# Kernel optimization log

Measured on AMD Instinct MI355X. Metric: run time of the kernel, lower is better.

Reference implementation:

```python
import jax, jax.numpy as jnp
import numpy as np

EPS = 1e-6


def sparsemax(z):
    # sparsemax over last axis (Martins & Astudillo 2016)
    n = z.shape[-1]
    zs = -jnp.sort(-z, axis=-1)                      # sorted descending
    cum = jnp.cumsum(zs, axis=-1)
    k = jnp.arange(1, n + 1, dtype=z.dtype)
    support = (1.0 + k * zs) > cum                   # [..., n]
    ksup = jnp.sum(support, axis=-1, keepdims=True)  # support size (int)
    tau = (jnp.take_along_axis(cum, ksup - 1, axis=-1) - 1.0) / ksup.astype(z.dtype)
    return jnp.maximum(z - tau, 0.0)


def setup_inputs() -> dict:
    key = jax.random.key(0)
    k1, k2, k3, k4, k5, k6 = jax.random.split(key, 6)
    bi, bt, K, L, d = 128, 128, 36, 50, 1024
    img_cls = jax.random.normal(k1, (bi, d), dtype=jnp.float32)
    imgs = jax.random.normal(k2, (bi, K, d), dtype=jnp.float32)
    cap_cls = jax.random.normal(k3, (bt, d), dtype=jnp.float32)
    caps = jax.random.normal(k4, (bt, L, d), dtype=jnp.float32)
    img_lens = jax.random.randint(k5, (bi,), 18, K + 1).at[0].set(K)
    cap_lens = jax.random.randint(k6, (bt,), 25, L + 1).at[0].set(L)
    return {"img_cls": img_cls, "imgs": imgs, "cap_cls": cap_cls,
            "caps": caps, "img_lens": img_lens, "cap_lens": cap_lens}


def reference(img_cls, imgs, cap_cls, caps, img_lens, cap_lens):
    # forward_s2d: masked fine-grained sims -> sparsemax over flattened (K*L) -> weighted sum
    bi, K, d = imgs.shape
    bt, L, _ = caps.shape
    imgs = imgs + EPS
    caps = caps + EPS
    imgs = imgs / jnp.linalg.norm(imgs, axis=-1, keepdims=True)
    caps = caps / jnp.linalg.norm(caps, axis=-1, keepdims=True)
    fg = jnp.einsum('ikd,tld->itkl', imgs, caps)             # [bi,bt,K,L]
    rmask = jnp.arange(K)[None, :] < img_lens[:, None]        # [bi,K]
    cmask = jnp.arange(L)[None, :] < cap_lens[:, None]        # [bt,L]
    mask = rmask[:, None, :, None] & cmask[None, :, None, :]  # [bi,bt,K,L]
    fg = jnp.where(mask, fg, 0.0).reshape(bi, bt, K * L)
    attn = sparsemax(fg)
    return jnp.sum(fg * attn, axis=-1)                        # [bi,bt]
```

## Files before the change

### kernel.cpp

```cpp
#include <hip/hip_runtime.h>
#include <stdint.h>

#define EPSF 1e-6f

typedef unsigned short u16;
typedef __attribute__((ext_vector_type(8))) u16 u16x8;
typedef __attribute__((ext_vector_type(8))) __bf16 bf16x8;
typedef __attribute__((ext_vector_type(4))) float f32x4;

static constexpr int NBI = 128, NBT = 128, KI = 36, LC = 50, DD = 1024;
static constexpr int NEL = KI * LC;
static constexpr int GM  = NBI * KI;
static constexpr int GN  = NBT * LC;
static constexpr int BM = 256, BN = 256, BK = 64;
static constexpr int KT  = DD / BK;
static constexpr int MT  = GM / BM;
static constexpr int NTT = GN / BN;
static constexpr int TB  = BM * BK;

static __device__ __forceinline__ u16 f2bf(float f) {
  uint32_t u = __float_as_uint(f);
  u += 0x7fffu + ((u >> 16) & 1u);
  return (u16)(u >> 16);
}
static __device__ __forceinline__ float bf2f(u16 h) {
  return __uint_as_float((uint32_t)h << 16);
}

typedef __attribute__((address_space(1))) void gv_t;
typedef __attribute__((address_space(3))) void lv_t;
static __device__ __forceinline__ void gload16(const void* g, void* l) {
  __builtin_amdgcn_global_load_lds((const gv_t*)g, (lv_t*)l, 16, 0, 0);
}

__global__ __launch_bounds__(256) void hcam_normcast(
    const float* __restrict__ imgs, const float* __restrict__ caps,
    u16* __restrict__ A, u16* __restrict__ B) {
  int r = blockIdx.x;
  const float* src; u16* dst;
  if (r < GM) { src = imgs + (size_t)r * DD;        dst = A + (size_t)r * DD; }
  else        { src = caps + (size_t)(r - GM) * DD; dst = B + (size_t)(r - GM) * DD; }
  int tid = threadIdx.x;
  float4 v = *(const float4*)(src + tid * 4);
  v.x += EPSF; v.y += EPSF; v.z += EPSF; v.w += EPSF;
  float ss = v.x * v.x + v.y * v.y + v.z * v.z + v.w * v.w;
  #pragma unroll
  for (int m = 32; m; m >>= 1) ss += __shfl_xor(ss, m);
  __shared__ float wsum[4];
  if ((tid & 63) == 0) wsum[tid >> 6] = ss;
  __syncthreads();
  float inv = 1.0f / sqrtf(wsum[0] + wsum[1] + wsum[2] + wsum[3]);
  ushort4 o = make_ushort4(f2bf(v.x * inv), f2bf(v.y * inv), f2bf(v.z * inv), f2bf(v.w * inv));
  *(ushort4*)(dst + tid * 4) = o;
}

__global__ __launch_bounds__(1024, 1) void hcam_gemm16(
    const u16* __restrict__ A, const u16* __restrict__ B, _Float16* __restrict__ C) {
  __shared__ u16 As[2 * TB];
  __shared__ u16 Bs[2 * TB];

  const int nwg = MT * NTT;
  int orig = blockIdx.x;
  int qq = nwg >> 3, rr = nwg & 7;
  int xcd = orig & 7, idx = orig >> 3;
  int wg = (xcd < rr ? xcd * (qq + 1) : rr * (qq + 1) + (xcd - rr) * qq) + idx;
  const int bm = wg % MT, bn = wg / MT;

  const int tid = threadIdx.x, lane = tid & 63, w = tid >> 6;
  const int wm = w >> 2, wn = w & 3;
  const u16* Ag = A + (size_t)(bm * BM) * DD;
  const u16* Bg = B + (size_t)(bn * BN) * DD;

  const int srow = tid >> 3;
  const int sc16 = (tid & 7) ^ (srow & 7);
  const int wbase = w * 8;

  auto stage = [&](const u16* g, u16* lds, int kt, int h) {
    gload16(g + (size_t)(h * 128 + srow) * DD + kt * BK + sc16 * 8,
            lds + (h * 128 + wbase) * BK);
  };

  f32x4 acc[4][4];
  #pragma unroll
  for (int i = 0; i < 4; ++i)
    #pragma unroll
    for (int j = 0; j < 4; ++j) acc[i][j] = (f32x4){0.f, 0.f, 0.f, 0.f};

  const int fr = lane & 15, g4 = lane >> 4;

  auto ktile_compute = [&](const u16* as_c, const u16* bs_c, bool st,
                           u16* as_n, u16* bs_n, int tn) {
    #pragma unroll
    for (int k2 = 0; k2 < 2; ++k2) {
      const int c16 = k2 * 4 + g4;
      const int cs = (c16 ^ (fr & 7)) << 3;
      bf16x8 af[4], bfv[4];
      #pragma unroll
      for (int mi = 0; mi < 4; ++mi) {
        int rowl = wm * 64 + mi * 16 + fr;
        af[mi] = __builtin_bit_cast(bf16x8, *(const u16x8*)(as_c + rowl * BK + cs));
      }
      #pragma unroll
      for (int ni = 0; ni < 4; ++ni) {
        int rowl = wn * 64 + ni * 16 + fr;
        bfv[ni] = __builtin_bit_cast(bf16x8, *(const u16x8*)(bs_c + rowl * BK + cs));
      }
      if (st) {
        if (k2 == 0) { stage(Bg, bs_n, tn, 0); }
        else         { stage(Ag, as_n, tn, 1); stage(Bg, bs_n, tn, 1); }
      }
      __builtin_amdgcn_s_setprio(1);
      #pragma unroll
      for (int mi = 0; mi < 4; ++mi)
        #pragma unroll
        for (int ni = 0; ni < 4; ++ni)
          acc[mi][ni] = __builtin_amdgcn_mfma_f32_16x16x32_bf16(
              af[mi], bfv[ni], acc[mi][ni], 0, 0, 0);
      __builtin_amdgcn_s_setprio(0);
    }
  };

  auto tile = [&](int t, const u16* as_c, const u16* bs_c, u16* as_n, u16* bs_n) {
    const int tn = t + 1;
    if (tn < KT) {
      stage(Ag, as_n, tn, 0);
      asm volatile("s_waitcnt vmcnt(1)" ::: "memory");
    } else {
      asm volatile("s_waitcnt vmcnt(0)" ::: "memory");
    }
    __builtin_amdgcn_s_barrier();
    __builtin_amdgcn_sched_barrier(0);
    ktile_compute(as_c, bs_c, tn < KT, as_n, bs_n, tn);
    __builtin_amdgcn_s_barrier();
    __builtin_amdgcn_sched_barrier(0);
  };

  stage(Ag, As, 0, 0); stage(Bg, Bs, 0, 0);
  stage(Ag, As, 0, 1); stage(Bg, Bs, 0, 1);
  stage(Ag, As + TB, 1, 0);
  asm volatile("s_waitcnt vmcnt(1)" ::: "memory");
  __builtin_amdgcn_s_barrier();
  __builtin_amdgcn_sched_barrier(0);
  ktile_compute(As, Bs, true, As + TB, Bs + TB, 1);
  __builtin_amdgcn_s_barrier();
  __builtin_amdgcn_sched_barrier(0);

  #pragma unroll 1
  for (int tp = 1; tp + 1 < KT; tp += 2) {
    tile(tp,     As + TB, Bs + TB, As,      Bs);
    tile(tp + 1, As,      Bs,      As + TB, Bs + TB);
  }
  tile(KT - 1, As + TB, Bs + TB, As, Bs);

  const int fc = lane & 15, fq = (lane >> 4) * 4;
  #pragma unroll
  for (int am = 0; am < 4; ++am) {
    #pragma unroll
    for (int an = 0; an < 4; ++an) {
      const int row0 = bm * BM + wm * 64 + am * 16 + fq;
      const int col  = bn * BN + wn * 64 + an * 16 + fc;
      #pragma unroll
      for (int j = 0; j < 4; ++j)
        C[(size_t)(row0 + j) * GN + col] = (_Float16)acc[am][an][j];
    }
  }
}

static constexpr int RPT = (NEL + 63) / 64;

__global__ __launch_bounds__(256) void hcam_spmax_w(
    const _Float16* __restrict__ C, const int* __restrict__ ilen, const int* __restrict__ clen,
    float* __restrict__ out) {
  const int wid  = blockIdx.x * 4 + (threadIdx.x >> 6);
  const int lane = threadIdx.x & 63;
  const int i = wid >> 7, t = wid & 127;
  const int il = ilen[i], cl = clen[t];
  const _Float16* base = C + (size_t)i * KI * GN + t * LC;

  float v[RPT];
  float sum = 0.f;
  #pragma unroll
  for (int r = 0; r < RPT; ++r) {
    int p = lane + (r << 6);
    float x = -1e30f;
    if (p < NEL) {
      int k = p / LC, l = p - k * LC;
      if (k < il && l < cl) { x = (float)base[(size_t)k * GN + l]; sum += x; }
    }
    v[r] = x;
  }
  #pragma unroll
  for (int m = 32; m; m >>= 1) sum += __shfl_xor(sum, m);

  const float mzero = (float)(NEL - il * cl);
  float tau  = (sum - 1.0f) * (1.0f / NEL);
  float prev = (float)NEL;
  for (int it = 0; it < 32; ++it) {
    float ss = 0.f, cc = 0.f;
    #pragma unroll
    for (int r = 0; r < RPT; ++r) {
      if (v[r] > tau) { ss += v[r]; cc += 1.0f; }
    }
    #pragma unroll
    for (int m = 32; m; m >>= 1) { ss += __shfl_xor(ss, m); cc += __shfl_xor(cc, m); }
    if (tau < 0.f) cc += mzero;
    if (cc == prev || cc < 1.0f) break;
    float tn = (ss - 1.0f) / cc;
    prev = cc;
    if (tn <= tau) break;
    tau = tn;
  }

  float o = 0.f;
  #pragma unroll
  for (int r = 0; r < RPT; ++r) {
    float d = v[r] - tau;
    if (d > 0.f) o += v[r] * d;
  }
  #pragma unroll
  for (int m = 32; m; m >>= 1) o += __shfl_xor(o, m);
  if (lane == 0) out[wid] = o;
}

static __device__ __forceinline__ void bred2(float& a, float& b2, int tid, float* red) {
  #pragma unroll
  for (int m = 32; m; m >>= 1) { a += __shfl_xor(a, m); b2 += __shfl_xor(b2, m); }
  __syncthreads();
  if ((tid & 63) == 0) { red[(tid >> 6) * 2] = a; red[(tid >> 6) * 2 + 1] = b2; }
  __syncthreads();
  a  = red[0] + red[2] + red[4] + red[6];
  b2 = red[1] + red[3] + red[5] + red[7];
}

static __device__ __forceinline__ void sparsemax_out(float vals[8], int tid, float* red, float* outp) {
  float s = 0.f, d = 0.f;
  #pragma unroll
  for (int r = 0; r < 8; ++r) { int p = tid + (r << 8); if (p < NEL) s += vals[r]; }
  bred2(s, d, tid, red);
  float tau  = (s - 1.0f) * (1.0f / NEL);
  float prev = (float)NEL;
  for (int it = 0; it < 64; ++it) {
    float ss = 0.f, cc = 0.f;
    #pragma unroll
    for (int r = 0; r < 8; ++r) {
      int p = tid + (r << 8);
      if (p < NEL && vals[r] > tau) { ss += vals[r]; cc += 1.0f; }
    }
    bred2(ss, cc, tid, red);
    if (cc == prev || cc < 1.0f) break;
    float tn = (ss - 1.0f) / cc;
    prev = cc;
    if (tn <= tau) break;
    tau = tn;
  }
  float o = 0.f; d = 0.f;
  #pragma unroll
  for (int r = 0; r < 8; ++r) {
    float v = vals[r], a2 = v - tau;
    if (a2 > 0.f) o += v * a2;
  }
  bred2(o, d, tid, red);
  if (tid == 0) *outp = o;
}

__global__ __launch_bounds__(256) void hcam_fused_bf(
    const u16* __restrict__ A, const u16* __restrict__ B,
    const int* __restrict__ ilen, const int* __restrict__ clen, float* __restrict__ out) {
  const int b = blockIdx.x;
  const int i = b >> 7, t = b & 127;
  const int tid = threadIdx.x;
  const int il = ilen[i], cl = clen[t];
  float vals[8];
  #pragma unroll
  for (int r = 0; r < 8; ++r) {
    int p = tid + (r << 8);
    float v = 0.f;
    if (p < NEL) {
      int k = p / LC, l = p - k * LC;
      if (k < il && l < cl) {
        const u16* ar = A + (size_t)(i * KI + k) * DD;
        const u16* br = B + (size_t)(t * LC + l) * DD;
        float s = 0.f;
        for (int dd = 0; dd < DD; dd += 8) {
          u16x8 av = *(const u16x8*)(ar + dd);
          u16x8 bv = *(const u16x8*)(br + dd);
          #pragma unroll
          for (int q = 0; q < 8; ++q) s += bf2f(av[q]) * bf2f(bv[q]);
        }
        v = s;
      }
    }
    vals[r] = v;
  }
  __shared__ float red[8];
  sparsemax_out(vals, tid, red, &out[b]);
}

__global__ __launch_bounds__(256) void hcam_fused_raw(
    const float* __restrict__ imgs, const float* __restrict__ caps,
    const int* __restrict__ ilen, const int* __restrict__ clen, float* __restrict__ out) {
  const int b = blockIdx.x;
  const int i = b >> 7, t = b & 127;
  const int tid = threadIdx.x;
  const int w = tid >> 6, lane = tid & 63;
  __shared__ float inv[KI + LC];
  for (int row = w; row < KI + LC; row += 4) {
    const float* src = (row < KI) ? imgs + (size_t)(i * KI + row) * DD
                                  : caps + (size_t)(t * LC + (row - KI)) * DD;
    float ss = 0.f;
    for (int e = lane; e < DD; e += 64) { float x = src[e] + EPSF; ss += x * x; }
    #pragma unroll
    for (int m = 32; m; m >>= 1) ss += __shfl_xor(ss, m);
    if (lane == 0) inv[row] = 1.0f / sqrtf(ss);
  }
  __syncthreads();
  const int il = ilen[i], cl = clen[t];
  float vals[8];
  #pragma unroll
  for (int r = 0; r < 8; ++r) {
    int p = tid + (r << 8);
    float v = 0.f;
    if (p < NEL) {
      int k = p / LC, l = p - k * LC;
      if (k < il && l < cl) {
        const float* ar = imgs + (size_t)(i * KI + k) * DD;
        const float* br = caps + (size_t)(t * LC + l) * DD;
        float s = 0.f;
        for (int dd = 0; dd < DD; dd += 4) {
          float4 a4 = *(const float4*)(ar + dd);
          float4 b4 = *(const float4*)(br + dd);
          s += (a4.x + EPSF) * (b4.x + EPSF) + (a4.y + EPSF) * (b4.y + EPSF)
             + (a4.z + EPSF) * (b4.z + EPSF) + (a4.w + EPSF) * (b4.w + EPSF);
        }
        v = s * inv[k] * inv[KI + l];
      }
    }
    vals[r] = v;
  }
  __shared__ float red[8];
  sparsemax_out(vals, tid, red, &out[b]);
}

extern "C" void kernel_launch(void* const* d_in, const int* in_sizes, int n_in,
                              void* d_out, int out_size, void* d_ws, size_t ws_size,
                              hipStream_t stream) {
  (void)in_sizes; (void)n_in; (void)out_size;
  const float* imgs = (const float*)d_in[1];
  const float* caps = (const float*)d_in[3];
  const int*   ilen = (const int*)d_in[4];
  const int*   clen = (const int*)d_in[5];
  float* out = (float*)d_out;

  const size_t offB     = (size_t)GM * DD * sizeof(u16);
  const size_t offC     = offB + (size_t)GN * DD * sizeof(u16);
  const size_t needFull = offC + (size_t)GM * GN * sizeof(_Float16);
  u16*      A = (u16*)d_ws;
  u16*      B = (u16*)((char*)d_ws + offB);
  _Float16* C = (_Float16*)((char*)d_ws + offC);

  if (ws_size >= needFull) {
    hcam_normcast<<<dim3(GM + GN), dim3(256), 0, stream>>>(imgs, caps, A, B);
    hcam_gemm16<<<dim3(MT * NTT), dim3(1024), 0, stream>>>(A, B, C);
    hcam_spmax_w<<<dim3(NBI * NBT / 4), dim3(256), 0, stream>>>(C, ilen, clen, out);
  } else if (ws_size >= offC) {
    hcam_normcast<<<dim3(GM + GN), dim3(256), 0, stream>>>(imgs, caps, A, B);
    hcam_fused_bf<<<dim3(NBI * NBT), dim3(256), 0, stream>>>(A, B, ilen, clen, out);
  } else {
    hcam_fused_raw<<<dim3(NBI * NBT), dim3(256), 0, stream>>>(imgs, caps, ilen, clen, out);
  }
}
```

Measured before the change: 126.8 us.

## Use 8-wave GEMM with 128x64 per-wave tiles and two blocks per CU

The bf16 GEMM moves from 16 waves of 64x64 output to 8 waves that each compute a 128x64 output sub-tile, with launch bounds set to allow two workgroups per CU. Each wave reuses its A and B fragments across more MFMAs, which lowers LDS read traffic per FLOP, and the global-to-LDS staging is spread across four interleaved phases within the k-tile. The cost is 128 accumulator registers per lane, which raises register pressure and could prevent two blocks from being resident. The LDS footprint per block is unchanged, so occupancy may stay limited by shared memory.

```diff
diff --git a/kernel.cpp b/kernel.cpp
--- a/kernel.cpp
+++ b/kernel.cpp
@@ -54,7 +54,7 @@
   *(ushort4*)(dst + tid * 4) = o;
 }
 
-__global__ __launch_bounds__(1024, 1) void hcam_gemm16(
+__global__ __launch_bounds__(512, 2) void hcam_gemm8r(
     const u16* __restrict__ A, const u16* __restrict__ B, _Float16* __restrict__ C) {
   __shared__ u16 As[2 * TB];
   __shared__ u16 Bs[2 * TB];
@@ -76,55 +76,104 @@
   const int wbase = w * 8;
 
   auto stage = [&](const u16* g, u16* lds, int kt, int h) {
-    gload16(g + (size_t)(h * 128 + srow) * DD + kt * BK + sc16 * 8,
-            lds + (h * 128 + wbase) * BK);
+    #pragma unroll
+    for (int j = 0; j < 2; ++j) {
+      int row = h * 128 + j * 64 + srow;
+      gload16(g + (size_t)row * DD + kt * BK + sc16 * 8,
+              lds + (h * 128 + j * 64 + wbase) * BK);
+    }
   };
 
-  f32x4 acc[4][4];
-  #pragma unroll
-  for (int i = 0; i < 4; ++i)
+  f32x4 acc[8][4];
+  #pragma unroll
+  for (int i = 0; i < 8; ++i)
     #pragma unroll
     for (int j = 0; j < 4; ++j) acc[i][j] = (f32x4){0.f, 0.f, 0.f, 0.f};
 
   const int fr = lane & 15, g4 = lane >> 4;
+
+  auto rdoff = [&](int rowl, int k2) {
+    const int c16 = k2 * 4 + g4;
+    return rowl * BK + ((c16 ^ (fr & 7)) << 3);
+  };
 
   auto ktile_compute = [&](const u16* as_c, const u16* bs_c, bool st,
                            u16* as_n, u16* bs_n, int tn) {
-    #pragma unroll
-    for (int k2 = 0; k2 < 2; ++k2) {
-      const int c16 = k2 * 4 + g4;
-      const int cs = (c16 ^ (fr & 7)) << 3;
-      bf16x8 af[4], bfv[4];
-      #pragma unroll
-      for (int mi = 0; mi < 4; ++mi) {
-        int rowl = wm * 64 + mi * 16 + fr;
-        af[mi] = __builtin_bit_cast(bf16x8, *(const u16x8*)(as_c + rowl * BK + cs));
-      }
-      #pragma unroll
-      for (int ni = 0; ni < 4; ++ni) {
-        int rowl = wn * 64 + ni * 16 + fr;
-        bfv[ni] = __builtin_bit_cast(bf16x8, *(const u16x8*)(bs_c + rowl * BK + cs));
-      }
-      if (st) {
-        if (k2 == 0) { stage(Bg, bs_n, tn, 0); }
-        else         { stage(Ag, as_n, tn, 1); stage(Bg, bs_n, tn, 1); }
-      }
-      __builtin_amdgcn_s_setprio(1);
+    bf16x8 af[4][2], blo[2][2], bhi[2][2];
+    #pragma unroll
+    for (int mi = 0; mi < 4; ++mi)
+      #pragma unroll
+      for (int k2 = 0; k2 < 2; ++k2)
+        af[mi][k2] = __builtin_bit_cast(bf16x8,
+            *(const u16x8*)(as_c + rdoff(wm * 128 + mi * 16 + fr, k2)));
+    #pragma unroll
+    for (int ni = 0; ni < 2; ++ni)
+      #pragma unroll
+      for (int k2 = 0; k2 < 2; ++k2)
+        blo[ni][k2] = __builtin_bit_cast(bf16x8,
+            *(const u16x8*)(bs_c + rdoff(wn * 64 + ni * 16 + fr, k2)));
+    if (st) stage(Bg, bs_n, tn, 0);
+    __builtin_amdgcn_s_setprio(1);
+    #pragma unroll
+    for (int k2 = 0; k2 < 2; ++k2)
       #pragma unroll
       for (int mi = 0; mi < 4; ++mi)
         #pragma unroll
-        for (int ni = 0; ni < 4; ++ni)
+        for (int ni = 0; ni < 2; ++ni)
           acc[mi][ni] = __builtin_amdgcn_mfma_f32_16x16x32_bf16(
-              af[mi], bfv[ni], acc[mi][ni], 0, 0, 0);
-      __builtin_amdgcn_s_setprio(0);
-    }
+              af[mi][k2], blo[ni][k2], acc[mi][ni], 0, 0, 0);
+    __builtin_amdgcn_s_setprio(0);
+    #pragma unroll
+    for (int ni = 0; ni < 2; ++ni)
+      #pragma unroll
+      for (int k2 = 0; k2 < 2; ++k2)
+        bhi[ni][k2] = __builtin_bit_cast(bf16x8,
+            *(const u16x8*)(bs_c + rdoff(wn * 64 + 32 + ni * 16 + fr, k2)));
+    if (st) stage(Ag, as_n, tn, 1);
+    __builtin_amdgcn_s_setprio(1);
+    #pragma unroll
+    for (int k2 = 0; k2 < 2; ++k2)
+      #pragma unroll
+      for (int mi = 0; mi < 4; ++mi)
+        #pragma unroll
+        for (int ni = 0; ni < 2; ++ni)
+          acc[mi][2 + ni] = __builtin_amdgcn_mfma_f32_16x16x32_bf16(
+              af[mi][k2], bhi[ni][k2], acc[mi][2 + ni], 0, 0, 0);
+    __builtin_amdgcn_s_setprio(0);
+    #pragma unroll
+    for (int mi = 0; mi < 4; ++mi)
+      #pragma unroll
+      for (int k2 = 0; k2 < 2; ++k2)
+        af[mi][k2] = __builtin_bit_cast(bf16x8,
+            *(const u16x8*)(as_c + rdoff(wm * 128 + 64 + mi * 16 + fr, k2)));
+    if (st) stage(Bg, bs_n, tn, 1);
+    __builtin_amdgcn_s_setprio(1);
+    #pragma unroll
+    for (int k2 = 0; k2 < 2; ++k2)
+      #pragma unroll
+      for (int mi = 0; mi < 4; ++mi)
+        #pragma unroll
+        for (int ni = 0; ni < 2; ++ni)
+          acc[4 + mi][ni] = __builtin_amdgcn_mfma_f32_16x16x32_bf16(
+              af[mi][k2], blo[ni][k2], acc[4 + mi][ni], 0, 0, 0);
+    __builtin_amdgcn_s_setprio(0);
+    __builtin_amdgcn_s_setprio(1);
+    #pragma unroll
+    for (int k2 = 0; k2 < 2; ++k2)
+      #pragma unroll
+      for (int mi = 0; mi < 4; ++mi)
+        #pragma unroll
+        for (int ni = 0; ni < 2; ++ni)
+          acc[4 + mi][2 + ni] = __builtin_amdgcn_mfma_f32_16x16x32_bf16(
+              af[mi][k2], bhi[ni][k2], acc[4 + mi][2 + ni], 0, 0, 0);
+    __builtin_amdgcn_s_setprio(0);
   };
 
   auto tile = [&](int t, const u16* as_c, const u16* bs_c, u16* as_n, u16* bs_n) {
     const int tn = t + 1;
     if (tn < KT) {
       stage(Ag, as_n, tn, 0);
-      asm volatile("s_waitcnt vmcnt(1)" ::: "memory");
+      asm volatile("s_waitcnt vmcnt(2)" ::: "memory");
     } else {
       asm volatile("s_waitcnt vmcnt(0)" ::: "memory");
     }
@@ -138,7 +187,7 @@
   stage(Ag, As, 0, 0); stage(Bg, Bs, 0, 0);
   stage(Ag, As, 0, 1); stage(Bg, Bs, 0, 1);
   stage(Ag, As + TB, 1, 0);
-  asm volatile("s_waitcnt vmcnt(1)" ::: "memory");
+  asm volatile("s_waitcnt vmcnt(2)" ::: "memory");
   __builtin_amdgcn_s_barrier();
   __builtin_amdgcn_sched_barrier(0);
   ktile_compute(As, Bs, true, As + TB, Bs + TB, 1);
@@ -154,16 +203,17 @@
 
   const int fc = lane & 15, fq = (lane >> 4) * 4;
   #pragma unroll
-  for (int am = 0; am < 4; ++am) {
-    #pragma unroll
-    for (int an = 0; an < 4; ++an) {
-      const int row0 = bm * BM + wm * 64 + am * 16 + fq;
-      const int col  = bn * BN + wn * 64 + an * 16 + fc;
-      #pragma unroll
-      for (int j = 0; j < 4; ++j)
-        C[(size_t)(row0 + j) * GN + col] = (_Float16)acc[am][an][j];
-    }
-  }
+  for (int mh = 0; mh < 2; ++mh)
+    #pragma unroll
+    for (int mi = 0; mi < 4; ++mi)
+      #pragma unroll
+      for (int an = 0; an < 4; ++an) {
+        const int row0 = bm * BM + wm * 128 + mh * 64 + mi * 16 + fq;
+        const int col  = bn * BN + wn * 64 + an * 16 + fc;
+        #pragma unroll
+        for (int j = 0; j < 4; ++j)
+          C[(size_t)(row0 + j) * GN + col] = (_Float16)acc[mh * 4 + mi][an][j];
+      }
 }
 
 static constexpr int RPT = (NEL + 63) / 64;
@@ -360,7 +410,7 @@
 
   if (ws_size >= needFull) {
     hcam_normcast<<<dim3(GM + GN), dim3(256), 0, stream>>>(imgs, caps, A, B);
-    hcam_gemm16<<<dim3(MT * NTT), dim3(1024), 0, stream>>>(A, B, C);
+    hcam_gemm8r<<<dim3(MT * NTT), dim3(512), 0, stream>>>(A, B, C);
     hcam_spmax_w<<<dim3(NBI * NBT / 4), dim3(256), 0, stream>>>(C, ilen, clen, out);
   } else if (ws_size >= offC) {
     hcam_normcast<<<dim3(GM + GN), dim3(256), 0, stream>>>(imgs, caps, A, B);
```

Result: no change. 124.6 us, median of 2 (-1.7%).

## Compact valid rows via prefix offsets and run GEMM only over valid tokens

Applied to the files above, without the earlier changes.

Adds a header kernel that prefix-sums image and caption lengths, then normalizes and writes only valid rows into compacted A/B buffers. The GEMM becomes a 128x128-tile, 256-thread kernel that covers only the compacted extents, skipping padded rows and columns and the matching C writes. The sparsemax kernel reads the compacted C with one lane per caption token. The cost is an extra serial single-thread launch, and the new GEMM is single-buffered with a full vmcnt(0) wait each k-step, so load and compute no longer overlap.

```diff
diff --git a/kernel.cpp b/kernel.cpp
--- a/kernel.cpp
+++ b/kernel.cpp
@@ -12,11 +12,8 @@
 static constexpr int NEL = KI * LC;
 static constexpr int GM  = NBI * KI;
 static constexpr int GN  = NBT * LC;
-static constexpr int BM = 256, BN = 256, BK = 64;
-static constexpr int KT  = DD / BK;
-static constexpr int MT  = GM / BM;
-static constexpr int NTT = GN / BN;
-static constexpr int TB  = BM * BK;
+static constexpr int BK = 64;
+static constexpr int KT = DD / BK;
 
 static __device__ __forceinline__ u16 f2bf(float f) {
   uint32_t u = __float_as_uint(f);
@@ -31,6 +28,182 @@
 typedef __attribute__((address_space(3))) void lv_t;
 static __device__ __forceinline__ void gload16(const void* g, void* l) {
   __builtin_amdgcn_global_load_lds((const gv_t*)g, (lv_t*)l, 16, 0, 0);
+}
+
+__global__ void hcam_hdr(const int* __restrict__ ilen, const int* __restrict__ clen,
+                         int* __restrict__ h) {
+  if (threadIdx.x == 0 && blockIdx.x == 0) {
+    int s = 0;
+    for (int i = 0; i < NBI; ++i) { h[8 + i] = s; s += ilen[i]; }
+    h[0] = s; h[1] = (s + 127) >> 7;
+    int s2 = 0;
+    for (int t = 0; t < NBT; ++t) { h[136 + t] = s2; s2 += clen[t]; }
+    h[2] = s2; h[3] = (s2 + 127) >> 7; h[4] = h[3] << 7;
+  }
+}
+
+__global__ __launch_bounds__(256) void hcam_normcast_c(
+    const float* __restrict__ imgs, const float* __restrict__ caps,
+    const int* __restrict__ ilen, const int* __restrict__ clen,
+    const int* __restrict__ h, u16* __restrict__ A, u16* __restrict__ B) {
+  int r = blockIdx.x;
+  const float* src; u16* dst;
+  if (r < GM) {
+    int i = r / KI, k = r - i * KI;
+    if (k >= ilen[i]) return;
+    src = imgs + (size_t)r * DD;
+    dst = A + (size_t)(h[8 + i] + k) * DD;
+  } else {
+    int rb = r - GM;
+    int t = rb / LC, l = rb - t * LC;
+    if (l >= clen[t]) return;
+    src = caps + (size_t)rb * DD;
+    dst = B + (size_t)(h[136 + t] + l) * DD;
+  }
+  int tid = threadIdx.x;
+  float4 v = *(const float4*)(src + tid * 4);
+  v.x += EPSF; v.y += EPSF; v.z += EPSF; v.w += EPSF;
+  float ss = v.x * v.x + v.y * v.y + v.z * v.z + v.w * v.w;
+  #pragma unroll
+  for (int m = 32; m; m >>= 1) ss += __shfl_xor(ss, m);
+  __shared__ float wsum[4];
+  if ((tid & 63) == 0) wsum[tid >> 6] = ss;
+  __syncthreads();
+  float inv = 1.0f / sqrtf(wsum[0] + wsum[1] + wsum[2] + wsum[3]);
+  ushort4 o = make_ushort4(f2bf(v.x * inv), f2bf(v.y * inv), f2bf(v.z * inv), f2bf(v.w * inv));
+  *(ushort4*)(dst + tid * 4) = o;
+}
+
+__global__ __launch_bounds__(256, 4) void hcam_gemm128(
+    const u16* __restrict__ A, const u16* __restrict__ B, _Float16* __restrict__ C,
+    const int* __restrict__ h) {
+  const int Mt = h[1], Nt = h[3], Npad = h[4];
+  const int orig = blockIdx.x;
+  const int wg = (orig & 7) * 225 + (orig >> 3);
+  const int bm = wg % 36, bn = wg / 36;
+  if (bm >= Mt || bn >= Nt) return;
+  __shared__ u16 As[128 * BK];
+  __shared__ u16 Bs[128 * BK];
+
+  const int tid = threadIdx.x, lane = tid & 63, w = tid >> 6;
+  const int wm = w >> 1, wn = w & 1;
+  const u16* Ag = A + (size_t)(bm * 128) * DD;
+  const u16* Bg = B + (size_t)(bn * 128) * DD;
+
+  const int srow = tid >> 3;
+  const int sc16 = (tid & 7) ^ (srow & 7);
+
+  f32x4 acc[4][4];
+  #pragma unroll
+  for (int i = 0; i < 4; ++i)
+    #pragma unroll
+    for (int j = 0; j < 4; ++j) acc[i][j] = (f32x4){0.f, 0.f, 0.f, 0.f};
+
+  const int fr = lane & 15, g4 = lane >> 4;
+
+  #pragma unroll 1
+  for (int kt = 0; kt < KT; ++kt) {
+    const int kb = kt * BK;
+    #pragma unroll
+    for (int j = 0; j < 4; ++j) {
+      const int row = j * 32 + srow;
+      const size_t gof = (size_t)row * DD + kb + sc16 * 8;
+      gload16(Ag + gof, As + (j * 32 + w * 8) * BK);
+      gload16(Bg + gof, Bs + (j * 32 + w * 8) * BK);
+    }
+    asm volatile("s_waitcnt vmcnt(0)" ::: "memory");
+    __builtin_amdgcn_s_barrier();
+
+    bf16x8 af[4][2], bfv[4][2];
+    #pragma unroll
+    for (int k2 = 0; k2 < 2; ++k2) {
+      const int cs = (((k2 << 2) + g4) ^ (fr & 7)) << 3;
+      #pragma unroll
+      for (int mi = 0; mi < 4; ++mi)
+        af[mi][k2] = __builtin_bit_cast(bf16x8,
+            *(const u16x8*)(As + (wm * 64 + mi * 16 + fr) * BK + cs));
+      #pragma unroll
+      for (int ni = 0; ni < 4; ++ni)
+        bfv[ni][k2] = __builtin_bit_cast(bf16x8,
+            *(const u16x8*)(Bs + (wn * 64 + ni * 16 + fr) * BK + cs));
+    }
+    __builtin_amdgcn_s_setprio(1);
+    #pragma unroll
+    for (int k2 = 0; k2 < 2; ++k2)
+      #pragma unroll
+      for (int mi = 0; mi < 4; ++mi)
+        #pragma unroll
+        for (int ni = 0; ni < 4; ++ni)
+          acc[mi][ni] = __builtin_amdgcn_mfma_f32_16x16x32_bf16(
+              af[mi][k2], bfv[ni][k2], acc[mi][ni], 0, 0, 0);
+    __builtin_amdgcn_s_setprio(0);
+    __builtin_amdgcn_s_barrier();
+  }
+
+  const int fc = lane & 15, fq = (lane >> 4) * 4;
+  #pragma unroll
+  for (int mi = 0; mi < 4; ++mi)
+    #pragma unroll
+    for (int ni = 0; ni < 4; ++ni) {
+      const int row0 = bm * 128 + wm * 64 + mi * 16 + fq;
+      const int col  = bn * 128 + wn * 64 + ni * 16 + fc;
+      #pragma unroll
+      for (int j = 0; j < 4; ++j)
+        C[(size_t)(row0 + j) * Npad + col] = (_Float16)acc[mi][ni][j];
+    }
+}
+
+__global__ __launch_bounds__(256) void hcam_spmax_w(
+    const _Float16* __restrict__ C, const int* __restrict__ ilen,
+    const int* __restrict__ clen, const int* __restrict__ h,
+    float* __restrict__ out) {
+  const int wid  = blockIdx.x * 4 + (threadIdx.x >> 6);
+  const int lane = threadIdx.x & 63;
+  const int i = wid >> 7, t = wid & 127;
+  const int il = ilen[i], cl = clen[t];
+  const int Npad = h[4];
+  const _Float16* base = C + (size_t)h[8 + i] * Npad + h[136 + t];
+
+  float v[KI];
+  float sum = 0.f;
+  const bool lv = lane < cl;
+  #pragma unroll
+  for (int r = 0; r < KI; ++r) {
+    float x = -1e30f;
+    if (r < il && lv) { x = (float)base[(size_t)r * Npad + lane]; sum += x; }
+    v[r] = x;
+  }
+  #pragma unroll
+  for (int m = 32; m; m >>= 1) sum += __shfl_xor(sum, m);
+
+  const float mzero = (float)(NEL - il * cl);
+  float tau  = (sum - 1.0f) * (1.0f / NEL);
+  float prev = (float)NEL;
+  for (int it = 0; it < 32; ++it) {
+    float ss = 0.f, cc = 0.f;
+    #pragma unroll
+    for (int r = 0; r < KI; ++r) {
+      if (v[r] > tau) { ss += v[r]; cc += 1.0f; }
+    }
+    #pragma unroll
+    for (int m = 32; m; m >>= 1) { ss += __shfl_xor(ss, m); cc += __shfl_xor(cc, m); }
+    if (tau < 0.f) cc += mzero;
+    if (cc == prev || cc < 1.0f) break;
+    float tn = (ss - 1.0f) / cc;
+    prev = cc;
+    if (tn <= tau) break;
+    tau = tn;
+  }
+
+  float o = 0.f;
+  #pragma unroll
+  for (int r = 0; r < KI; ++r) {
+    float d = v[r] - tau;
+    if (d > 0.f) o += v[r] * d;
+  }
+  #pragma unroll
+  for (int m = 32; m; m >>= 1) o += __shfl_xor(o, m);
+  if (lane == 0) out[wid] = o;
 }
 
 __global__ __launch_bounds__(256) void hcam_normcast(
@@ -52,174 +225,6 @@
   float inv = 1.0f / sqrtf(wsum[0] + wsum[1] + wsum[2] + wsum[3]);
   ushort4 o = make_ushort4(f2bf(v.x * inv), f2bf(v.y * inv), f2bf(v.z * inv), f2bf(v.w * inv));
   *(ushort4*)(dst + tid * 4) = o;
-}
-
-__global__ __launch_bounds__(1024, 1) void hcam_gemm16(
-    const u16* __restrict__ A, const u16* __restrict__ B, _Float16* __restrict__ C) {
-  __shared__ u16 As[2 * TB];
-  __shared__ u16 Bs[2 * TB];
-
-  const int nwg = MT * NTT;
-  int orig = blockIdx.x;
-  int qq = nwg >> 3, rr = nwg & 7;
-  int xcd = orig & 7, idx = orig >> 3;
-  int wg = (xcd < rr ? xcd * (qq + 1) : rr * (qq + 1) + (xcd - rr) * qq) + idx;
-  const int bm = wg % MT, bn = wg / MT;
-
-  const int tid = threadIdx.x, lane = tid & 63, w = tid >> 6;
-  const int wm = w >> 2, wn = w & 3;
-  const u16* Ag = A + (size_t)(bm * BM) * DD;
-  const u16* Bg = B + (size_t)(bn * BN) * DD;
-
-  const int srow = tid >> 3;
-  const int sc16 = (tid & 7) ^ (srow & 7);
-  const int wbase = w * 8;
-
-  auto stage = [&](const u16* g, u16* lds, int kt, int h) {
-    gload16(g + (size_t)(h * 128 + srow) * DD + kt * BK + sc16 * 8,
-            lds + (h * 128 + wbase) * BK);
-  };
-
-  f32x4 acc[4][4];
-  #pragma unroll
-  for (int i = 0; i < 4; ++i)
-    #pragma unroll
-    for (int j = 0; j < 4; ++j) acc[i][j] = (f32x4){0.f, 0.f, 0.f, 0.f};
-
-  const int fr = lane & 15, g4 = lane >> 4;
-
-  auto ktile_compute = [&](const u16* as_c, const u16* bs_c, bool st,
-                           u16* as_n, u16* bs_n, int tn) {
-    #pragma unroll
-    for (int k2 = 0; k2 < 2; ++k2) {
-      const int c16 = k2 * 4 + g4;
-      const int cs = (c16 ^ (fr & 7)) << 3;
-      bf16x8 af[4], bfv[4];
-      #pragma unroll
-      for (int mi = 0; mi < 4; ++mi) {
-        int rowl = wm * 64 + mi * 16 + fr;
-        af[mi] = __builtin_bit_cast(bf16x8, *(const u16x8*)(as_c + rowl * BK + cs));
-      }
-      #pragma unroll
-      for (int ni = 0; ni < 4; ++ni) {
-        int rowl = wn * 64 + ni * 16 + fr;
-        bfv[ni] = __builtin_bit_cast(bf16x8, *(const u16x8*)(bs_c + rowl * BK + cs));
-      }
-      if (st) {
-        if (k2 == 0) { stage(Bg, bs_n, tn, 0); }
-        else         { stage(Ag, as_n, tn, 1); stage(Bg, bs_n, tn, 1); }
-      }
-      __builtin_amdgcn_s_setprio(1);
-      #pragma unroll
-      for (int mi = 0; mi < 4; ++mi)
-        #pragma unroll
-        for (int ni = 0; ni < 4; ++ni)
-          acc[mi][ni] = __builtin_amdgcn_mfma_f32_16x16x32_bf16(
-              af[mi], bfv[ni], acc[mi][ni], 0, 0, 0);
-      __builtin_amdgcn_s_setprio(0);
-    }
-  };
-
-  auto tile = [&](int t, const u16* as_c, const u16* bs_c, u16* as_n, u16* bs_n) {
-    const int tn = t + 1;
-    if (tn < KT) {
-      stage(Ag, as_n, tn, 0);
-      asm volatile("s_waitcnt vmcnt(1)" ::: "memory");
-    } else {
-      asm volatile("s_waitcnt vmcnt(0)" ::: "memory");
-    }
-    __builtin_amdgcn_s_barrier();
-    __builtin_amdgcn_sched_barrier(0);
-    ktile_compute(as_c, bs_c, tn < KT, as_n, bs_n, tn);
-    __builtin_amdgcn_s_barrier();
-    __builtin_amdgcn_sched_barrier(0);
-  };
-
-  stage(Ag, As, 0, 0); stage(Bg, Bs, 0, 0);
-  stage(Ag, As, 0, 1); stage(Bg, Bs, 0, 1);
-  stage(Ag, As + TB, 1, 0);
-  asm volatile("s_waitcnt vmcnt(1)" ::: "memory");
-  __builtin_amdgcn_s_barrier();
-  __builtin_amdgcn_sched_barrier(0);
-  ktile_compute(As, Bs, true, As + TB, Bs + TB, 1);
-  __builtin_amdgcn_s_barrier();
-  __builtin_amdgcn_sched_barrier(0);
-
-  #pragma unroll 1
-  for (int tp = 1; tp + 1 < KT; tp += 2) {
-    tile(tp,     As + TB, Bs + TB, As,      Bs);
-    tile(tp + 1, As,      Bs,      As + TB, Bs + TB);
-  }
-  tile(KT - 1, As + TB, Bs + TB, As, Bs);
-
-  const int fc = lane & 15, fq = (lane >> 4) * 4;
-  #pragma unroll
-  for (int am = 0; am < 4; ++am) {
-    #pragma unroll
-    for (int an = 0; an < 4; ++an) {
-      const int row0 = bm * BM + wm * 64 + am * 16 + fq;
-      const int col  = bn * BN + wn * 64 + an * 16 + fc;
-      #pragma unroll
-      for (int j = 0; j < 4; ++j)
-        C[(size_t)(row0 + j) * GN + col] = (_Float16)acc[am][an][j];
-    }
-  }
-}
-
-static constexpr int RPT = (NEL + 63) / 64;
-
-__global__ __launch_bounds__(256) void hcam_spmax_w(
-    const _Float16* __restrict__ C, const int* __restrict__ ilen, const int* __restrict__ clen,
-    float* __restrict__ out) {
-  const int wid  = blockIdx.x * 4 + (threadIdx.x >> 6);
-  const int lane = threadIdx.x & 63;
-  const int i = wid >> 7, t = wid & 127;
-  const int il = ilen[i], cl = clen[t];
-  const _Float16* base = C + (size_t)i * KI * GN + t * LC;
-
-  float v[RPT];
-  float sum = 0.f;
-  #pragma unroll
-  for (int r = 0; r < RPT; ++r) {
-    int p = lane + (r << 6);
-    float x = -1e30f;
-    if (p < NEL) {
-      int k = p / LC, l = p - k * LC;
-      if (k < il && l < cl) { x = (float)base[(size_t)k * GN + l]; sum += x; }
-    }
-    v[r] = x;
-  }
-  #pragma unroll
-  for (int m = 32; m; m >>= 1) sum += __shfl_xor(sum, m);
-
-  const float mzero = (float)(NEL - il * cl);
-  float tau  = (sum - 1.0f) * (1.0f / NEL);
-  float prev = (float)NEL;
-  for (int it = 0; it < 32; ++it) {
-    float ss = 0.f, cc = 0.f;
-    #pragma unroll
-    for (int r = 0; r < RPT; ++r) {
-      if (v[r] > tau) { ss += v[r]; cc += 1.0f; }
-    }
-    #pragma unroll
-    for (int m = 32; m; m >>= 1) { ss += __shfl_xor(ss, m); cc += __shfl_xor(cc, m); }
-    if (tau < 0.f) cc += mzero;
-    if (cc == prev || cc < 1.0f) break;
-    float tn = (ss - 1.0f) / cc;
-    prev = cc;
-    if (tn <= tau) break;
-    tau = tn;
-  }
-
-  float o = 0.f;
-  #pragma unroll
-  for (int r = 0; r < RPT; ++r) {
-    float d = v[r] - tau;
-    if (d > 0.f) o += v[r] * d;
-  }
-  #pragma unroll
-  for (int m = 32; m; m >>= 1) o += __shfl_xor(o, m);
-  if (lane == 0) out[wid] = o;
 }
 
 static __device__ __forceinline__ void bred2(float& a, float& b2, int tid, float* red) {
@@ -351,17 +356,20 @@
   const int*   clen = (const int*)d_in[5];
   float* out = (float*)d_out;
 
-  const size_t offB     = (size_t)GM * DD * sizeof(u16);
+  const size_t offA     = 4096;
+  const size_t offB     = offA + (size_t)GM * DD * sizeof(u16);
   const size_t offC     = offB + (size_t)GN * DD * sizeof(u16);
   const size_t needFull = offC + (size_t)GM * GN * sizeof(_Float16);
-  u16*      A = (u16*)d_ws;
+  int*      hdr = (int*)d_ws;
+  u16*      A = (u16*)((char*)d_ws + offA);
   u16*      B = (u16*)((char*)d_ws + offB);
   _Float16* C = (_Float16*)((char*)d_ws + offC);
 
   if (ws_size >= needFull) {
-    hcam_normcast<<<dim3(GM + GN), dim3(256), 0, stream>>>(imgs, caps, A, B);
-    hcam_gemm16<<<dim3(MT * NTT), dim3(1024), 0, stream>>>(A, B, C);
-    hcam_spmax_w<<<dim3(NBI * NBT / 4), dim3(256), 0, stream>>>(C, ilen, clen, out);
+    hcam_hdr<<<dim3(1), dim3(64), 0, stream>>>(ilen, clen, hdr);
+    hcam_normcast_c<<<dim3(GM + GN), dim3(256), 0, stream>>>(imgs, caps, ilen, clen, hdr, A, B);
+    hcam_gemm128<<<dim3(36 * 50), dim3(256), 0, stream>>>(A, B, C, hdr);
+    hcam_spmax_w<<<dim3(NBI * NBT / 4), dim3(256), 0, stream>>>(C, ilen, clen, hdr, out);
   } else if (ws_size >= offC) {
     hcam_normcast<<<dim3(GM + GN), dim3(256), 0, stream>>>(imgs, caps, A, B);
     hcam_fused_bf<<<dim3(NBI * NBT), dim3(256), 0, stream>>>(A, B, ilen, clen, out);
```

New measurement: 201.2 us. 1.59x slower.

## Switch GEMM to 128x128x32 tiles with 256-thread blocks and 4 blocks per CU

Applied to the files above, without the earlier changes.

Replaces the 256x256x64 single-block-per-CU GEMM with a 128x128x32 tile kernel using 4 waves and up to 4 resident blocks per CU. The staging pattern, LDS swizzle and XCD remapping are rewritten to match (8 XCDs x 225 tiles). The aim is more workgroups for better load balance across CUs and more occupancy to hide latency. The cost is lower operand reuse per tile, so more global and LDS traffic, plus more barriers per unit of work.

```diff
diff --git a/kernel.cpp b/kernel.cpp
--- a/kernel.cpp
+++ b/kernel.cpp
@@ -12,11 +12,11 @@
 static constexpr int NEL = KI * LC;
 static constexpr int GM  = NBI * KI;
 static constexpr int GN  = NBT * LC;
-static constexpr int BM = 256, BN = 256, BK = 64;
-static constexpr int KT  = DD / BK;
-static constexpr int MT  = GM / BM;
-static constexpr int NTT = GN / BN;
-static constexpr int TB  = BM * BK;
+static constexpr int BM = 128, BN = 128, BK = 32;
+static constexpr int KT = DD / BK;
+static constexpr int MT = GM / BM;
+static constexpr int NT = GN / BN;
+static constexpr int TBA = BM * BK;
 
 static __device__ __forceinline__ u16 f2bf(float f) {
   uint32_t u = __float_as_uint(f);
@@ -54,30 +54,30 @@
   *(ushort4*)(dst + tid * 4) = o;
 }
 
-__global__ __launch_bounds__(1024, 1) void hcam_gemm16(
+__global__ __launch_bounds__(256, 4) void hcam_gemm128d(
     const u16* __restrict__ A, const u16* __restrict__ B, _Float16* __restrict__ C) {
-  __shared__ u16 As[2 * TB];
-  __shared__ u16 Bs[2 * TB];
-
-  const int nwg = MT * NTT;
-  int orig = blockIdx.x;
-  int qq = nwg >> 3, rr = nwg & 7;
-  int xcd = orig & 7, idx = orig >> 3;
-  int wg = (xcd < rr ? xcd * (qq + 1) : rr * (qq + 1) + (xcd - rr) * qq) + idx;
+  __shared__ u16 As[2 * TBA];
+  __shared__ u16 Bs[2 * TBA];
+
+  const int orig = blockIdx.x;
+  const int wg = (orig & 7) * 225 + (orig >> 3);
   const int bm = wg % MT, bn = wg / MT;
 
   const int tid = threadIdx.x, lane = tid & 63, w = tid >> 6;
-  const int wm = w >> 2, wn = w & 3;
+  const int wm = w >> 1, wn = w & 1;
   const u16* Ag = A + (size_t)(bm * BM) * DD;
   const u16* Bg = B + (size_t)(bn * BN) * DD;
 
-  const int srow = tid >> 3;
-  const int sc16 = (tid & 7) ^ (srow & 7);
-  const int wbase = w * 8;
-
-  auto stage = [&](const u16* g, u16* lds, int kt, int h) {
-    gload16(g + (size_t)(h * 128 + srow) * DD + kt * BK + sc16 * 8,
-            lds + (h * 128 + wbase) * BK);
+  const int sc4 = (tid & 3) ^ ((tid >> 3) & 3);
+  const int srow = tid >> 2;
+
+  auto stage = [&](const u16* g, u16* lds, int kt) {
+    #pragma unroll
+    for (int j = 0; j < 2; ++j) {
+      int row = j * 64 + srow;
+      gload16(g + (size_t)row * DD + kt * BK + sc4 * 8,
+              lds + (j * 64 + w * 16) * BK);
+    }
   };
 
   f32x4 acc[4][4];
@@ -87,83 +87,71 @@
     for (int j = 0; j < 4; ++j) acc[i][j] = (f32x4){0.f, 0.f, 0.f, 0.f};
 
   const int fr = lane & 15, g4 = lane >> 4;
-
-  auto ktile_compute = [&](const u16* as_c, const u16* bs_c, bool st,
-                           u16* as_n, u16* bs_n, int tn) {
-    #pragma unroll
-    for (int k2 = 0; k2 < 2; ++k2) {
-      const int c16 = k2 * 4 + g4;
-      const int cs = (c16 ^ (fr & 7)) << 3;
-      bf16x8 af[4], bfv[4];
+  const int cs = ((g4 ^ ((fr >> 1) & 3)) << 3);
+
+  auto ktile_compute = [&](const u16* as_c, const u16* bs_c, bool st, u16* bs_n, int tn) {
+    bf16x8 af[4], bfv[4];
+    #pragma unroll
+    for (int mi = 0; mi < 4; ++mi)
+      af[mi] = __builtin_bit_cast(bf16x8,
+          *(const u16x8*)(as_c + (wm * 64 + mi * 16 + fr) * BK + cs));
+    #pragma unroll
+    for (int ni = 0; ni < 4; ++ni)
+      bfv[ni] = __builtin_bit_cast(bf16x8,
+          *(const u16x8*)(bs_c + (wn * 64 + ni * 16 + fr) * BK + cs));
+    if (st) stage(Bg, bs_n, tn);
+    __builtin_amdgcn_s_setprio(1);
+    #pragma unroll
+    for (int mi = 0; mi < 4; ++mi)
       #pragma unroll
-      for (int mi = 0; mi < 4; ++mi) {
-        int rowl = wm * 64 + mi * 16 + fr;
-        af[mi] = __builtin_bit_cast(bf16x8, *(const u16x8*)(as_c + rowl * BK + cs));
-      }
-      #pragma unroll
-      for (int ni = 0; ni < 4; ++ni) {
-        int rowl = wn * 64 + ni * 16 + fr;
-        bfv[ni] = __builtin_bit_cast(bf16x8, *(const u16x8*)(bs_c + rowl * BK + cs));
-      }
-      if (st) {
-        if (k2 == 0) { stage(Bg, bs_n, tn, 0); }
-        else         { stage(Ag, as_n, tn, 1); stage(Bg, bs_n, tn, 1); }
-      }
-      __builtin_amdgcn_s_setprio(1);
-      #pragma unroll
-      for (int mi = 0; mi < 4; ++mi)
-        #pragma unroll
-        for (int ni = 0; ni < 4; ++ni)
-          acc[mi][ni] = __builtin_amdgcn_mfma_f32_16x16x32_bf16(
-              af[mi], bfv[ni], acc[mi][ni], 0, 0, 0);
-      __builtin_amdgcn_s_setprio(0);
-    }
+      for (int ni = 0; ni < 4; ++ni)
+        acc[mi][ni] = __builtin_amdgcn_mfma_f32_16x16x32_bf16(
+            af[mi], bfv[ni], acc[mi][ni], 0, 0, 0);
+    __builtin_amdgcn_s_setprio(0);
   };
 
   auto tile = [&](int t, const u16* as_c, const u16* bs_c, u16* as_n, u16* bs_n) {
     const int tn = t + 1;
     if (tn < KT) {
-      stage(Ag, as_n, tn, 0);
-      asm volatile("s_waitcnt vmcnt(1)" ::: "memory");
+      stage(Ag, as_n, tn);
+      asm volatile("s_waitcnt vmcnt(2)" ::: "memory");
     } else {
       asm volatile("s_waitcnt vmcnt(0)" ::: "memory");
     }
     __builtin_amdgcn_s_barrier();
     __builtin_amdgcn_sched_barrier(0);
-    ktile_compute(as_c, bs_c, tn < KT, as_n, bs_n, tn);
+    ktile_compute(as_c, bs_c, tn < KT, bs_n, tn);
     __builtin_amdgcn_s_barrier();
     __builtin_amdgcn_sched_barrier(0);
   };
 
-  stage(Ag, As, 0, 0); stage(Bg, Bs, 0, 0);
-  stage(Ag, As, 0, 1); stage(Bg, Bs, 0, 1);
-  stage(Ag, As + TB, 1, 0);
-  asm volatile("s_waitcnt vmcnt(1)" ::: "memory");
+  stage(Ag, As, 0); stage(Bg, Bs, 0);
+  stage(Ag, As + TBA, 1);
+  asm volatile("s_waitcnt vmcnt(2)" ::: "memory");
   __builtin_amdgcn_s_barrier();
   __builtin_amdgcn_sched_barrier(0);
-  ktile_compute(As, Bs, true, As + TB, Bs + TB, 1);
+  ktile_compute(As, Bs, true, Bs + TBA, 1);
   __builtin_amdgcn_s_barrier();
   __builtin_amdgcn_sched_barrier(0);
 
   #pragma unroll 1
   for (int tp = 1; tp + 1 < KT; tp += 2) {
-    tile(tp,     As + TB, Bs + TB, As,      Bs);
-    tile(tp + 1, As,      Bs,      As + TB, Bs + TB);
-  }
-  tile(KT - 1, As + TB, Bs + TB, As, Bs);
+    tile(tp,     As + TBA, Bs + TBA, As,       Bs);
+    tile(tp + 1, As,       Bs,       As + TBA, Bs + TBA);
+  }
+  tile(KT - 1, As + TBA, Bs + TBA, As, Bs);
 
   const int fc = lane & 15, fq = (lane >> 4) * 4;
   #pragma unroll
-  for (int am = 0; am < 4; ++am) {
-    #pragma unroll
-    for (int an = 0; an < 4; ++an) {
-      const int row0 = bm * BM + wm * 64 + am * 16 + fq;
-      const int col  = bn * BN + wn * 64 + an * 16 + fc;
+  for (int mi = 0; mi < 4; ++mi)
+    #pragma unroll
+    for (int ni = 0; ni < 4; ++ni) {
+      const int row0 = bm * BM + wm * 64 + mi * 16 + fq;
+      const int col  = bn * BN + wn * 64 + ni * 16 + fc;
       #pragma unroll
       for (int j = 0; j < 4; ++j)
-        C[(size_t)(row0 + j) * GN + col] = (_Float16)acc[am][an][j];
-    }
-  }
+        C[(size_t)(row0 + j) * GN + col] = (_Float16)acc[mi][ni][j];
+    }
 }
 
 static constexpr int RPT = (NEL + 63) / 64;
@@ -360,7 +348,7 @@
 
   if (ws_size >= needFull) {
     hcam_normcast<<<dim3(GM + GN), dim3(256), 0, stream>>>(imgs, caps, A, B);
-    hcam_gemm16<<<dim3(MT * NTT), dim3(1024), 0, stream>>>(A, B, C);
+    hcam_gemm128d<<<dim3(MT * NT), dim3(256), 0, stream>>>(A, B, C);
     hcam_spmax_w<<<dim3(NBI * NBT / 4), dim3(256), 0, stream>>>(C, ilen, clen, out);
   } else if (ws_size >= offC) {
     hcam_normcast<<<dim3(GM + GN), dim3(256), 0, stream>>>(imgs, caps, A, B);
```

New measurement: 137.2 us. 8.2% more time.
